# Performance work log

Measured on AMD Instinct MI355X. Metric: run time of the kernel, lower is better.

The kernel has to match this reference:

```python
import jax, jax.numpy as jnp
import numpy as np

EPS = 1e-5
NUM_HEAD = 8
HEAD_DIM = 64
SCALE = HEAD_DIM ** -0.5


def setup_inputs() -> dict:
    key = jax.random.key(0)
    ks = jax.random.split(key, 3)
    b, n, dim = 4, 2048, 512
    inner = NUM_HEAD * HEAD_DIM  # 512
    x = jax.random.normal(ks[0], (b, n, dim), dtype=jnp.float32)
    ln_w = jnp.ones((dim,), jnp.float32)
    ln_b = jnp.zeros((dim,), jnp.float32)
    qkv_w = jax.random.normal(ks[1], (3 * inner, dim), jnp.float32) * (dim ** -0.5)
    qkv_b = jnp.zeros((3 * inner,), jnp.float32)
    out_w = jax.random.normal(ks[2], (dim, inner), jnp.float32) * (inner ** -0.5)
    out_b = jnp.zeros((dim,), jnp.float32)
    return {"x": x, "ln_w": ln_w, "ln_b": ln_b, "qkv_w": qkv_w,
            "qkv_b": qkv_b, "out_w": out_w, "out_b": out_b}


def reference(x, ln_w, ln_b, qkv_w, qkv_b, out_w, out_b):
    b, n, dim = x.shape
    # Pre-norm LayerNorm
    mu = jnp.mean(x, axis=-1, keepdims=True)
    var = jnp.mean(jnp.square(x - mu), axis=-1, keepdims=True)
    xn = (x - mu) * jax.lax.rsqrt(var + EPS) * ln_w + ln_b
    # QKV projection (torch Linear: y = x @ W.T + b)
    qkv = xn @ qkv_w.T + qkv_b  # [b, n, 3*inner]
    q, k, v = jnp.split(qkv, 3, axis=-1)
    def heads(t):  # [b, n, inner] -> [b, h, n, d]
        return t.reshape(b, n, NUM_HEAD, HEAD_DIM).transpose(0, 2, 1, 3)
    q, k, v = heads(q), heads(k), heads(v)
    # Naive full attention (materializes [b, h, n, n])
    dots = jnp.einsum('bhqd,bhkd->bhqk', q, k) * SCALE
    attn = jax.nn.softmax(dots, axis=-1)
    o = jnp.einsum('bhqk,bhkd->bhqd', attn, v)
    o = o.transpose(0, 2, 1, 3).reshape(b, n, NUM_HEAD * HEAD_DIM)
    return o @ out_w.T + out_b
```

## Files before the change

### kernel.cpp

```cpp
#include <hip/hip_runtime.h>

typedef __attribute__((ext_vector_type(8))) short bf16x8;
typedef __attribute__((ext_vector_type(4))) float floatx4;
typedef __attribute__((ext_vector_type(16))) float floatx16;
typedef __attribute__((ext_vector_type(4))) unsigned int uintx4;

#define B_    4
#define N_    2048
#define DIM_  512
#define NH_   8
#define HD_   64
#define SCALE_ 0.125f
#define SL2E_ (0.125f * 1.44269504f)

__device__ __forceinline__ unsigned short f32_to_bf16(float f) {
    return (unsigned short)((__float_as_uint(f) + 0x8000u) >> 16);
}

__device__ __forceinline__ float bf16_to_f32(unsigned short u) {
    return __uint_as_float(((unsigned int)u) << 16);
}

__device__ __forceinline__ floatx4 mfma16(bf16x8 a, bf16x8 b, floatx4 c) {
    return __builtin_amdgcn_mfma_f32_16x16x32_bf16(a, b, c, 0, 0, 0);
}

__device__ __forceinline__ floatx16 mfma32(bf16x8 a, bf16x8 b, floatx16 c) {
    return __builtin_amdgcn_mfma_f32_32x32x16_bf16(a, b, c, 0, 0, 0);
}

__device__ __forceinline__ floatx4 fzero4() {
    floatx4 z = {0.f, 0.f, 0.f, 0.f};
    return z;
}

__device__ __forceinline__ floatx16 fzero16() {
    floatx16 z;
#pragma unroll
    for (int i = 0; i < 16; i++) z[i] = 0.f;
    return z;
}

__device__ __forceinline__ unsigned int cvt_pk_bf16(float lo, float hi) {
    unsigned int r;
    asm("v_cvt_pk_bf16_f32 %0, %1, %2" : "=v"(r) : "v"(lo), "v"(hi));
    return r;
}

__device__ __forceinline__ void async16(const unsigned short* g, unsigned short* l) {
    __builtin_amdgcn_global_load_lds((const __attribute__((address_space(1))) void*)g,
                                     (__attribute__((address_space(3))) void*)l,
                                     16, 0, 0);
}

__global__ __launch_bounds__(256) void ln_cvt_kernel(const float* __restrict__ x,
                                                     const float* __restrict__ w,
                                                     const float* __restrict__ b,
                                                     unsigned short* __restrict__ xn,
                                                     const float* __restrict__ srcA,
                                                     const float* __restrict__ srcB,
                                                     unsigned short* __restrict__ dstA,
                                                     unsigned short* __restrict__ dstB) {
    const int NWQ = 3 * DIM_ * DIM_;
    if (blockIdx.x < 2048) {
        int wv = threadIdx.x >> 6;
        int lane = threadIdx.x & 63;
        int row = blockIdx.x * 4 + wv;
        const float4* xr = (const float4*)(x + (size_t)row * DIM_);
        float4 v0 = xr[lane * 2];
        float4 v1 = xr[lane * 2 + 1];
        float s  = (v0.x + v0.y + v0.z + v0.w) + (v1.x + v1.y + v1.z + v1.w);
        float sq = v0.x*v0.x + v0.y*v0.y + v0.z*v0.z + v0.w*v0.w +
                   v1.x*v1.x + v1.y*v1.y + v1.z*v1.z + v1.w*v1.w;
#pragma unroll
        for (int off = 1; off < 64; off <<= 1) {
            s  += __shfl_xor(s, off, 64);
            sq += __shfl_xor(sq, off, 64);
        }
        float mu   = s * (1.f / DIM_);
        float var  = sq * (1.f / DIM_) - mu * mu;
        float rstd = rsqrtf(var + 1e-5f);
        float4 w0 = ((const float4*)w)[lane * 2];
        float4 w1 = ((const float4*)w)[lane * 2 + 1];
        float4 b0 = ((const float4*)b)[lane * 2];
        float4 b1 = ((const float4*)b)[lane * 2 + 1];
        float y[8];
        y[0] = (v0.x - mu) * rstd * w0.x + b0.x;
        y[1] = (v0.y - mu) * rstd * w0.y + b0.y;
        y[2] = (v0.z - mu) * rstd * w0.z + b0.z;
        y[3] = (v0.w - mu) * rstd * w0.w + b0.w;
        y[4] = (v1.x - mu) * rstd * w1.x + b1.x;
        y[5] = (v1.y - mu) * rstd * w1.y + b1.y;
        y[6] = (v1.z - mu) * rstd * w1.z + b1.z;
        y[7] = (v1.w - mu) * rstd * w1.w + b1.w;
        uint4 pk;
        pk.x = (unsigned int)f32_to_bf16(y[0]) | ((unsigned int)f32_to_bf16(y[1]) << 16);
        pk.y = (unsigned int)f32_to_bf16(y[2]) | ((unsigned int)f32_to_bf16(y[3]) << 16);
        pk.z = (unsigned int)f32_to_bf16(y[4]) | ((unsigned int)f32_to_bf16(y[5]) << 16);
        pk.w = (unsigned int)f32_to_bf16(y[6]) | ((unsigned int)f32_to_bf16(y[7]) << 16);
        ((uint4*)(xn + (size_t)row * DIM_))[lane] = pk;
    } else {
        int e0 = ((blockIdx.x - 2048) * 256 + threadIdx.x) * 8;
        const float* src;
        unsigned short* dst;
        if (e0 < NWQ) { src = srcA + e0; dst = dstA + e0; }
        else          { src = srcB + (e0 - NWQ); dst = dstB + (e0 - NWQ); }
        float4 u0 = ((const float4*)src)[0];
        float4 u1 = ((const float4*)src)[1];
        uint4 pk;
        pk.x = (unsigned int)f32_to_bf16(u0.x) | ((unsigned int)f32_to_bf16(u0.y) << 16);
        pk.y = (unsigned int)f32_to_bf16(u0.z) | ((unsigned int)f32_to_bf16(u0.w) << 16);
        pk.z = (unsigned int)f32_to_bf16(u1.x) | ((unsigned int)f32_to_bf16(u1.y) << 16);
        pk.w = (unsigned int)f32_to_bf16(u1.z) | ((unsigned int)f32_to_bf16(u1.w) << 16);
        *(uint4*)dst = pk;
    }
}

#define GEMM_CORE512(A_, B_ptr, am0, bn0)                                           \
    __shared__ unsigned short Alds[2][128][32];                                     \
    __shared__ unsigned short Blds[2][128][32];                                     \
    int tid = threadIdx.x, lane = tid & 63, wid = tid >> 6;                         \
    int l15 = lane & 15, quad = lane >> 4;                                          \
    int wmloc = (wid >> 1) * 32, wnloc = (wid & 1) * 64;                            \
    int sr = lane >> 2;                                                             \
    int sc = (lane & 3) * 8;                                                        \
    int srow0 = 16 * wid;                                                           \
    floatx4 acc[2][4];                                                              \
    _Pragma("unroll")                                                               \
    for (int i = 0; i < 2; i++)                                                     \
        _Pragma("unroll")                                                           \
        for (int j = 0; j < 4; j++) acc[i][j] = fzero4();                           \
    int buf = 0;                                                                    \
    async16(A_ + (size_t)(am0 + srow0 + sr) * DIM_ + sc, &Alds[0][srow0][0]);       \
    async16(B_ptr + (size_t)(bn0 + srow0 + sr) * DIM_ + sc, &Blds[0][srow0][0]);    \
    __syncthreads();                                                                \
    for (int t = 0; t < 16; t++) {                                                  \
        if (t < 15) {                                                               \
            int k0 = (t + 1) * 32;                                                  \
            async16(A_ + (size_t)(am0 + srow0 + sr) * DIM_ + k0 + sc,               \
                    &Alds[buf ^ 1][srow0][0]);                                      \
            async16(B_ptr + (size_t)(bn0 + srow0 + sr) * DIM_ + k0 + sc,            \
                    &Blds[buf ^ 1][srow0][0]);                                      \
        }                                                                           \
        bf16x8 av[2], bv[4];                                                        \
        _Pragma("unroll")                                                           \
        for (int i = 0; i < 2; i++)                                                 \
            av[i] = *(const bf16x8*)(&Alds[buf][wmloc + 16 * i + l15][quad * 8]);   \
        _Pragma("unroll")                                                           \
        for (int j = 0; j < 4; j++)                                                 \
            bv[j] = *(const bf16x8*)(&Blds[buf][wnloc + 16 * j + l15][quad * 8]);   \
        _Pragma("unroll")                                                           \
        for (int i = 0; i < 2; i++)                                                 \
            _Pragma("unroll")                                                       \
            for (int j = 0; j < 4; j++)                                             \
                acc[i][j] = mfma16(av[i], bv[j], acc[i][j]);                        \
        __syncthreads();                                                            \
        buf ^= 1;                                                                   \
    }

__global__ __launch_bounds__(512, 6) void qkv_gemm(const unsigned short* __restrict__ A,
                                                   const unsigned short* __restrict__ Bw,
                                                   const float* __restrict__ bias,
                                                   unsigned short* __restrict__ Qh,
                                                   unsigned short* __restrict__ Kh,
                                                   unsigned short* __restrict__ Vt) {
    int am0 = blockIdx.x * 128, bn0 = blockIdx.y * 128;
    GEMM_CORE512(A, Bw, am0, bn0)

    if (bn0 >= 1024) {
        unsigned short* sc_ = &Alds[0][0][0] + wid * (16 * 40);
        int m0 = am0 + wmloc;
        int bidx = m0 >> 11;
        int t0 = m0 & 2047;
#pragma unroll
        for (int j = 0; j < 4; j++) {
            float bias_n = bias[bn0 + wnloc + 16 * j + l15];
#pragma unroll
            for (int i = 0; i < 2; i++)
#pragma unroll
                for (int r = 0; r < 4; r++)
                    sc_[l15 * 40 + 16 * i + quad * 4 + r] =
                        f32_to_bf16(acc[i][j][r] + bias_n);
            int nr = lane >> 2;
            int rem = (bn0 - 1024) + wnloc + 16 * j + nr;
            int head = rem >> 6, d = rem & 63;
            bf16x8 vv = *(const bf16x8*)(sc_ + nr * 40 + (lane & 3) * 8);
            *(bf16x8*)(Vt + ((size_t)(bidx * NH_ + head) * HD_ + d) * N_ +
                       t0 + (lane & 3) * 8) = vv;
        }
    } else {
        unsigned short* sc2 = &Alds[0][0][0] + wid * 1024;
        int n0 = bn0 + wnloc;
        int which = n0 >> 9;
        int head = (n0 & 511) >> 6;
        unsigned short* dstBase = (which == 0) ? Qh : Kh;
        float mul = (which == 0) ? SL2E_ : 1.f;
#pragma unroll
        for (int i = 0; i < 2; i++) {
#pragma unroll
            for (int j = 0; j < 4; j++) {
                float bias_n = bias[n0 + 16 * j + l15];
#pragma unroll
                for (int r = 0; r < 4; r++)
                    sc2[(quad * 4 + r) * 64 + 16 * j + l15] =
                        f32_to_bf16((acc[i][j][r] + bias_n) * mul);
            }
            asm volatile("s_waitcnt lgkmcnt(0)" ::: "memory");
#pragma unroll
            for (int h = 0; h < 2; h++) {
                int tl = 8 * h + (lane >> 3);
                int m = am0 + wmloc + 16 * i + tl;
                int bb2 = m >> 11, tt = m & 2047;
                bf16x8 row = *(const bf16x8*)(sc2 + tl * 64 + (lane & 7) * 8);
                *(bf16x8*)(dstBase + ((size_t)(bb2 * NH_ + head) * N_ + tt) * HD_ +
                           (lane & 7) * 8) = row;
            }
        }
    }
}

__global__ __launch_bounds__(256, 4) void out_gemm_fused(const unsigned short* __restrict__ Opart,
                                                         const float* __restrict__ lpart,
                                                         const unsigned short* __restrict__ Bw,
                                                         const float* __restrict__ bias,
                                                         float* __restrict__ out) {
    __shared__ unsigned short Alds[2][64][36];
    __shared__ unsigned short Blds[2][128][32];
    int tid = threadIdx.x, lane = tid & 63, wid = tid >> 6;
    int l15 = lane & 15, quad = lane >> 4;
    int wmloc = (wid >> 1) * 32, wnloc = (wid & 1) * 64;
    int am0 = blockIdx.x * 64, bn0 = blockIdx.y * 128;

    int arow = tid >> 2;
    int ac8 = (tid & 3) * 8;
    int token = am0 + arow;
    int bb = token >> 11;
    const size_t LSTR = (size_t)B_ * NH_ * N_;
    const size_t OSTR = (size_t)B_ * N_ * DIM_;
    const unsigned short* arow0 = Opart + (size_t)token * DIM_;
    const unsigned short* arow1 = arow0 + OSTR;

    int sr = lane >> 2;
    int sc = (lane & 3) * 8;

    floatx4 acc[2][4];
#pragma unroll
    for (int i = 0; i < 2; i++)
#pragma unroll
        for (int j = 0; j < 4; j++) acc[i][j] = fzero4();

#define STAGE_A(BUF, T)                                                         \
    {                                                                           \
        int k0 = (T) * 32;                                                      \
        int head = k0 >> 6;                                                     \
        size_t li = (size_t)(bb * NH_ + head) * N_ + (token & 2047);            \
        float l1 = lpart[li];                                                   \
        float l2 = lpart[LSTR + li];                                            \
        float inv = 1.f / (l1 + l2);                                            \
        float w1 = l1 * inv, w2 = l2 * inv;                                     \
        bf16x8 o0 = *(const bf16x8*)(arow0 + k0 + ac8);                         \
        bf16x8 o1 = *(const bf16x8*)(arow1 + k0 + ac8);                         \
        bf16x8 pk;                                                              \
        _Pragma("unroll")                                                       \
        for (int e = 0; e < 8; e++)                                             \
            pk[e] = (short)f32_to_bf16(                                         \
                w1 * bf16_to_f32((unsigned short)o0[e]) +                       \
                w2 * bf16_to_f32((unsigned short)o1[e]));                       \
        *(bf16x8*)(&Alds[BUF][arow][ac8]) = pk;                                 \
    }

#define STAGE_B(BUF, T)                                                         \
    {                                                                           \
        int k0 = (T) * 32;                                                      \
        _Pragma("unroll")                                                       \
        for (int i = 0; i < 2; i++) {                                           \
            int r0 = 32 * wid + 16 * i;                                         \
            async16(Bw + (size_t)(bn0 + r0 + sr) * DIM_ + k0 + sc,              \
                    &Blds[BUF][r0][0]);                                         \
        }                                                                       \
    }

    STAGE_B(0, 0)
    STAGE_A(0, 0)
    __syncthreads();
    int buf = 0;
    for (int t = 0; t < 16; t++) {
        if (t < 15) {
            STAGE_B(buf ^ 1, t + 1)
            STAGE_A(buf ^ 1, t + 1)
        }
        bf16x8 av[2], bv[4];
#pragma unroll
        for (int i = 0; i < 2; i++)
            av[i] = *(const bf16x8*)(&Alds[buf][wmloc + 16 * i + l15][quad * 8]);
#pragma unroll
        for (int j = 0; j < 4; j++)
            bv[j] = *(const bf16x8*)(&Blds[buf][wnloc + 16 * j + l15][quad * 8]);
#pragma unroll
        for (int i = 0; i < 2; i++)
#pragma unroll
            for (int j = 0; j < 4; j++)
                acc[i][j] = mfma16(av[i], bv[j], acc[i][j]);
        __syncthreads();
        buf ^= 1;
    }
#undef STAGE_A
#undef STAGE_B

#pragma unroll
    for (int i = 0; i < 2; i++) {
#pragma unroll
        for (int j = 0; j < 4; j++) {
            int n = bn0 + wnloc + 16 * j + l15;
            float bias_n = bias[n];
#pragma unroll
            for (int r = 0; r < 4; r++) {
                int m = am0 + wmloc + 16 * i + quad * 4 + r;
                out[(size_t)m * DIM_ + n] = acc[i][j][r] + bias_n;
            }
        }
    }
}

__global__ __launch_bounds__(256, 4) void attn_kernel(const unsigned short* __restrict__ Qh,
                                                      const unsigned short* __restrict__ Kh,
                                                      const unsigned short* __restrict__ Vtg,
                                                      unsigned short* __restrict__ Opart,
                                                      float* __restrict__ lpart) {
    int bh = blockIdx.y;
    int b = bh >> 3, head = bh & 7;
    int qt = blockIdx.x;
    int split = blockIdx.z;
    int kv0 = split << 10;
    int tid = threadIdx.x, lane = tid & 63, w = tid >> 6;
    int l31 = lane & 31, hi = lane >> 5;
    int xr = l31 & 7;

    const unsigned short* Qp = Qh + (size_t)bh * N_ * HD_;
    const unsigned short* Kg = Kh + (size_t)bh * N_ * HD_;
    const unsigned short* Vg = Vtg + (size_t)bh * HD_ * N_;

    int q0 = qt * 128 + w * 32;

    bf16x8 aQ[4];
    {
        const unsigned short* qrow = Qp + (size_t)(q0 + l31) * HD_ + hi * 8;
#pragma unroll
        for (int t = 0; t < 4; t++)
            aQ[t] = *(const bf16x8*)(qrow + 16 * t);
    }

    __shared__ unsigned short KV[2][2][64][64];

    int srow = lane >> 3;
    int scol = ((lane & 7) ^ srow) * 8;

    const char* ptc[4];
#pragma unroll
    for (int t = 0; t < 4; t++)
        ptc[t] = (const char*)&KV[0][0][l31][(((2 * t + hi) ^ xr) * 8)];

    const unsigned short* kSrc = Kg + (size_t)(kv0 + 16 * w + srow) * HD_ + scol;
    const unsigned short* vSrc = Vg + (size_t)(16 * w + srow) * N_ + kv0 + scol;

#define STAGE_KV(BUF, IT)                                                       \
    {                                                                           \
        _Pragma("unroll")                                                       \
        for (int i = 0; i < 2; i++) {                                           \
            int r0 = 16 * w + 8 * i;                                            \
            async16(kSrc + (size_t)(IT) * 64 * HD_ + i * 8 * HD_,               \
                    &KV[BUF][0][r0][0]);                                        \
            async16(vSrc + (size_t)(IT) * 64 + i * 8 * N_,                      \
                    &KV[BUF][1][r0][0]);                                        \
        }                                                                       \
    }

    floatx16 of[2];
    of[0] = fzero16();
    of[1] = fzero16();
    floatx16 lacc = fzero16();
    const floatx16 z16 = fzero16();

    const short onebf = (short)0x3F80;
    bf16x8 onesB = {onebf, onebf, onebf, onebf, onebf, onebf, onebf, onebf};

#define COMPUTE(BUF)                                                            \
    {                                                                           \
        bf16x8 pa[4];                                                           \
        _Pragma("unroll")                                                       \
        for (int tau = 0; tau < 2; tau++) {                                     \
            bf16x8 kf[4];                                                       \
            _Pragma("unroll")                                                   \
            for (int t = 0; t < 4; t++)                                         \
                kf[t] = *(const bf16x8*)(ptc[t] + (BUF) * 16384 + tau * 4096);  \
            __builtin_amdgcn_s_setprio(1);                                      \
            floatx16 acc = mfma32(kf[0], aQ[0], z16);                           \
            acc = mfma32(kf[1], aQ[1], acc);                                    \
            acc = mfma32(kf[2], aQ[2], acc);                                    \
            acc = mfma32(kf[3], aQ[3], acc);                                    \
            __builtin_amdgcn_s_setprio(0);                                      \
            float p[16];                                                        \
            _Pragma("unroll")                                                   \
            for (int r = 0; r < 16; r++)                                        \
                p[r] = __builtin_amdgcn_exp2f(acc[r]);                          \
            unsigned int a0 = cvt_pk_bf16(p[0], p[1]);                          \
            unsigned int b0 = cvt_pk_bf16(p[4], p[5]);                          \
            unsigned int a1 = cvt_pk_bf16(p[2], p[3]);                          \
            unsigned int b1 = cvt_pk_bf16(p[6], p[7]);                          \
            unsigned int a2 = cvt_pk_bf16(p[8], p[9]);                          \
            unsigned int b2 = cvt_pk_bf16(p[12], p[13]);                        \
            unsigned int a3 = cvt_pk_bf16(p[10], p[11]);                        \
            unsigned int b3 = cvt_pk_bf16(p[14], p[15]);                        \
            asm("v_permlane32_swap_b32 %0, %1" : "+v"(a0), "+v"(b0));           \
            asm("v_permlane32_swap_b32 %0, %1" : "+v"(a1), "+v"(b1));           \
            asm("v_permlane32_swap_b32 %0, %1" : "+v"(a2), "+v"(b2));           \
            asm("v_permlane32_swap_b32 %0, %1" : "+v"(a3), "+v"(b3));           \
            uintx4 f0 = {a0, a1, b0, b1};                                       \
            uintx4 f1 = {a2, a3, b2, b3};                                       \
            pa[2 * tau]     = __builtin_bit_cast(bf16x8, f0);                   \
            pa[2 * tau + 1] = __builtin_bit_cast(bf16x8, f1);                   \
        }                                                                       \
        __builtin_amdgcn_s_setprio(1);                                          \
        _Pragma("unroll")                                                       \
        for (int s = 0; s < 4; s++) {                                           \
            _Pragma("unroll")                                                   \
            for (int dt = 0; dt < 2; dt++) {                                    \
                bf16x8 vf = *(const bf16x8*)(ptc[s] + (BUF) * 16384 + 8192 +    \
                                             dt * 4096);                        \
                of[dt] = mfma32(pa[s], vf, of[dt]);                             \
            }                                                                   \
            lacc = mfma32(pa[s], onesB, lacc);                                  \
        }                                                                       \
        __builtin_amdgcn_s_setprio(0);                                          \
    }

    STAGE_KV(0, 0)
    __syncthreads();

    for (int it2 = 0; it2 < 8; it2++) {
        int it = it2 * 2;
        STAGE_KV(1, it + 1)
        COMPUTE(0)
        __syncthreads();
        if (it2 < 7) STAGE_KV(0, it + 2)
        COMPUTE(1)
        __syncthreads();
    }
#undef STAGE_KV
#undef COMPUTE

    unsigned short* Od = Opart + (size_t)split * B_ * N_ * DIM_;
#pragma unroll
    for (int r = 0; r < 16; r++) {
        int qr = (r & 3) + 8 * (r >> 2) + 4 * hi;
        float inv = __builtin_amdgcn_rcpf(lacc[r]);
        int token = q0 + qr;
        size_t base = ((size_t)b * N_ + token) * DIM_ + (size_t)head * HD_;
#pragma unroll
        for (int dt = 0; dt < 2; dt++)
            Od[base + 32 * dt + l31] = f32_to_bf16(of[dt][r] * inv);
    }
    if (l31 == 0) {
#pragma unroll
        for (int r = 0; r < 16; r++) {
            int qr = (r & 3) + 8 * (r >> 2) + 4 * hi;
            lpart[(size_t)split * B_ * NH_ * N_ + (size_t)bh * N_ + q0 + qr] =
                lacc[r];
        }
    }
}

extern "C" void kernel_launch(void* const* d_in, const int* in_sizes, int n_in,
                              void* d_out, int out_size, void* d_ws, size_t ws_size,
                              hipStream_t stream) {
    const float* x     = (const float*)d_in[0];
    const float* ln_w  = (const float*)d_in[1];
    const float* ln_b  = (const float*)d_in[2];
    const float* qkv_w = (const float*)d_in[3];
    const float* qkv_b = (const float*)d_in[4];
    const float* out_w = (const float*)d_in[5];
    const float* out_b = (const float*)d_in[6];
    float* out = (float*)d_out;

    char* ws = (char*)d_ws;
    const size_t TOK = (size_t)B_ * N_;
    unsigned short* xn    = (unsigned short*)ws;  ws += TOK * DIM_ * 2;
    unsigned short* wq_bf = (unsigned short*)ws;  ws += (size_t)3 * DIM_ * DIM_ * 2;
    unsigned short* wo_bf = (unsigned short*)ws;  ws += (size_t)DIM_ * DIM_ * 2;
    unsigned short* Qh    = (unsigned short*)ws;  ws += TOK * DIM_ * 2;
    unsigned short* Kh    = (unsigned short*)ws;  ws += TOK * DIM_ * 2;
    unsigned short* Vt    = (unsigned short*)ws;  ws += TOK * DIM_ * 2;
    unsigned short* Opart = (unsigned short*)ws;  ws += (size_t)2 * TOK * DIM_ * 2;
    float*          lpart = (float*)ws;           ws += (size_t)2 * B_ * NH_ * N_ * 4;

    ln_cvt_kernel<<<2048 + 512, 256, 0, stream>>>(x, ln_w, ln_b, xn,
                                                  qkv_w, out_w, wq_bf, wo_bf);
    qkv_gemm<<<dim3(TOK / 128, (3 * DIM_) / 128), 512, 0, stream>>>(xn, wq_bf, qkv_b, Qh, Kh, Vt);
    attn_kernel<<<dim3(N_ / 128, B_ * NH_, 2), 256, 0, stream>>>(Qh, Kh, Vt, Opart, lpart);
    out_gemm_fused<<<dim3(TOK / 64, DIM_ / 128), 256, 0, stream>>>(Opart, lpart, wo_bf, out_b, out);
}
```

Before: 156.5 us.

## Split split-K combine out of output GEMM and reuse 512-thread GEMM core

Removes the fused combine-plus-GEMM kernel. A separate elementwise kernel now merges the two attention partial outputs into a bf16 buffer, and the output projection uses the shared 128x128, 512-thread GEMM core also used for QKV. The goal is to stop redoing the combine work in every N-tile block (four times per element) and to get the more efficient pipelined GEMM. The cost is an extra kernel launch plus an extra write and read of an 8 MB intermediate.

```diff
diff --git a/kernel.cpp b/kernel.cpp
--- a/kernel.cpp
+++ b/kernel.cpp
@@ -219,93 +219,38 @@
     }
 }
 
-__global__ __launch_bounds__(256, 4) void out_gemm_fused(const unsigned short* __restrict__ Opart,
-                                                         const float* __restrict__ lpart,
-                                                         const unsigned short* __restrict__ Bw,
-                                                         const float* __restrict__ bias,
-                                                         float* __restrict__ out) {
-    __shared__ unsigned short Alds[2][64][36];
-    __shared__ unsigned short Blds[2][128][32];
-    int tid = threadIdx.x, lane = tid & 63, wid = tid >> 6;
-    int l15 = lane & 15, quad = lane >> 4;
-    int wmloc = (wid >> 1) * 32, wnloc = (wid & 1) * 64;
-    int am0 = blockIdx.x * 64, bn0 = blockIdx.y * 128;
-
-    int arow = tid >> 2;
-    int ac8 = (tid & 3) * 8;
-    int token = am0 + arow;
-    int bb = token >> 11;
+__global__ __launch_bounds__(256) void combine_kernel(const unsigned short* __restrict__ Opart,
+                                                      const float* __restrict__ lpart,
+                                                      unsigned short* __restrict__ Oc) {
+    int idx = blockIdx.x * 256 + threadIdx.x;
+    int tok = idx >> 6;
+    int c8 = idx & 63;
+    int head = c8 >> 3;
     const size_t LSTR = (size_t)B_ * NH_ * N_;
     const size_t OSTR = (size_t)B_ * N_ * DIM_;
-    const unsigned short* arow0 = Opart + (size_t)token * DIM_;
-    const unsigned short* arow1 = arow0 + OSTR;
-
-    int sr = lane >> 2;
-    int sc = (lane & 3) * 8;
-
-    floatx4 acc[2][4];
-#pragma unroll
-    for (int i = 0; i < 2; i++)
-#pragma unroll
-        for (int j = 0; j < 4; j++) acc[i][j] = fzero4();
-
-#define STAGE_A(BUF, T)                                                         \
-    {                                                                           \
-        int k0 = (T) * 32;                                                      \
-        int head = k0 >> 6;                                                     \
-        size_t li = (size_t)(bb * NH_ + head) * N_ + (token & 2047);            \
-        float l1 = lpart[li];                                                   \
-        float l2 = lpart[LSTR + li];                                            \
-        float inv = 1.f / (l1 + l2);                                            \
-        float w1 = l1 * inv, w2 = l2 * inv;                                     \
-        bf16x8 o0 = *(const bf16x8*)(arow0 + k0 + ac8);                         \
-        bf16x8 o1 = *(const bf16x8*)(arow1 + k0 + ac8);                         \
-        bf16x8 pk;                                                              \
-        _Pragma("unroll")                                                       \
-        for (int e = 0; e < 8; e++)                                             \
-            pk[e] = (short)f32_to_bf16(                                         \
-                w1 * bf16_to_f32((unsigned short)o0[e]) +                       \
-                w2 * bf16_to_f32((unsigned short)o1[e]));                       \
-        *(bf16x8*)(&Alds[BUF][arow][ac8]) = pk;                                 \
-    }
-
-#define STAGE_B(BUF, T)                                                         \
-    {                                                                           \
-        int k0 = (T) * 32;                                                      \
-        _Pragma("unroll")                                                       \
-        for (int i = 0; i < 2; i++) {                                           \
-            int r0 = 32 * wid + 16 * i;                                         \
-            async16(Bw + (size_t)(bn0 + r0 + sr) * DIM_ + k0 + sc,              \
-                    &Blds[BUF][r0][0]);                                         \
-        }                                                                       \
-    }
-
-    STAGE_B(0, 0)
-    STAGE_A(0, 0)
-    __syncthreads();
-    int buf = 0;
-    for (int t = 0; t < 16; t++) {
-        if (t < 15) {
-            STAGE_B(buf ^ 1, t + 1)
-            STAGE_A(buf ^ 1, t + 1)
-        }
-        bf16x8 av[2], bv[4];
-#pragma unroll
-        for (int i = 0; i < 2; i++)
-            av[i] = *(const bf16x8*)(&Alds[buf][wmloc + 16 * i + l15][quad * 8]);
-#pragma unroll
-        for (int j = 0; j < 4; j++)
-            bv[j] = *(const bf16x8*)(&Blds[buf][wnloc + 16 * j + l15][quad * 8]);
-#pragma unroll
-        for (int i = 0; i < 2; i++)
-#pragma unroll
-            for (int j = 0; j < 4; j++)
-                acc[i][j] = mfma16(av[i], bv[j], acc[i][j]);
-        __syncthreads();
-        buf ^= 1;
-    }
-#undef STAGE_A
-#undef STAGE_B
+    int b = tok >> 11, t = tok & 2047;
+    size_t li = (size_t)(b * NH_ + head) * N_ + t;
+    float l1 = lpart[li];
+    float l2 = lpart[LSTR + li];
+    float inv = 1.f / (l1 + l2);
+    float w1 = l1 * inv, w2 = l2 * inv;
+    const unsigned short* p0 = Opart + (size_t)tok * DIM_ + c8 * 8;
+    bf16x8 o0 = *(const bf16x8*)(p0);
+    bf16x8 o1 = *(const bf16x8*)(p0 + OSTR);
+    bf16x8 pk;
+#pragma unroll
+    for (int e = 0; e < 8; e++)
+        pk[e] = (short)f32_to_bf16(w1 * bf16_to_f32((unsigned short)o0[e]) +
+                                   w2 * bf16_to_f32((unsigned short)o1[e]));
+    *(bf16x8*)(Oc + (size_t)tok * DIM_ + c8 * 8) = pk;
+}
+
+__global__ __launch_bounds__(512, 6) void out_gemm(const unsigned short* __restrict__ A,
+                                                   const unsigned short* __restrict__ Bw,
+                                                   const float* __restrict__ bias,
+                                                   float* __restrict__ out) {
+    int am0 = blockIdx.x * 128, bn0 = blockIdx.y * 128;
+    GEMM_CORE512(A, Bw, am0, bn0)
 
 #pragma unroll
     for (int i = 0; i < 2; i++) {
@@ -491,11 +436,13 @@
     unsigned short* Kh    = (unsigned short*)ws;  ws += TOK * DIM_ * 2;
     unsigned short* Vt    = (unsigned short*)ws;  ws += TOK * DIM_ * 2;
     unsigned short* Opart = (unsigned short*)ws;  ws += (size_t)2 * TOK * DIM_ * 2;
+    unsigned short* Oc    = (unsigned short*)ws;  ws += TOK * DIM_ * 2;
     float*          lpart = (float*)ws;           ws += (size_t)2 * B_ * NH_ * N_ * 4;
 
     ln_cvt_kernel<<<2048 + 512, 256, 0, stream>>>(x, ln_w, ln_b, xn,
                                                   qkv_w, out_w, wq_bf, wo_bf);
     qkv_gemm<<<dim3(TOK / 128, (3 * DIM_) / 128), 512, 0, stream>>>(xn, wq_bf, qkv_b, Qh, Kh, Vt);
     attn_kernel<<<dim3(N_ / 128, B_ * NH_, 2), 256, 0, stream>>>(Qh, Kh, Vt, Opart, lpart);
-    out_gemm_fused<<<dim3(TOK / 64, DIM_ / 128), 256, 0, stream>>>(Opart, lpart, wo_bf, out_b, out);
-}
+    combine_kernel<<<(int)(TOK * DIM_ / 8 / 256), 256, 0, stream>>>(Opart, lpart, Oc);
+    out_gemm<<<dim3(TOK / 128, DIM_ / 128), 512, 0, stream>>>(Oc, wo_bf, out_b, out);
+}
```

Measured after the change: 160.3 us. 2.4% more time.
